# Kernel tuning notes

Measured on AMD Instinct MI355X. Metric: run time of the kernel, lower is better.

Reference implementation:

```python
import jax, jax.numpy as jnp
import numpy as np

N = 64
DX0 = np.pi / N
B = 4096
N_ENV = 8
CODE = 128


def setup_inputs() -> dict:
    key = jax.random.key(0)
    k1, k2, k3 = jax.random.split(key, 3)
    y0 = jax.random.normal(k1, (B, 1, N, N), dtype=jnp.float32)
    env = jax.random.randint(k2, (B,), 0, N_ENV).astype(jnp.int64)
    codes = jax.random.normal(k3, (B, CODE), dtype=jnp.float32)
    t = jnp.zeros((1,), dtype=jnp.float32)
    # learned params: [mu, domain_placeholder] per env (matches nn.Parameter init)
    params = jnp.concatenate([jnp.full((N_ENV, 1), 0.005, jnp.float32),
                              jnp.full((N_ENV, 1), 1.0, jnp.float32)], axis=1)
    # fixed domain buffer for n_env == 8
    domain = jnp.array([0.75, 1.0, 0.75, 1.0, 0.75, 1.0, 0.75, 1.0],
                       dtype=jnp.float32)[:, None]  # [n_env, 1]
    return {"t": t, "y0": y0, "env": env, "codes": codes,
            "params": params, "domain": domain}


def _dx(a):  # roll along last axis (torch dims=2 on [B,H,W])
    return jnp.roll(a, -1, axis=2) - jnp.roll(a, 1, axis=2)


def _dy(a):  # roll along axis 1
    return jnp.roll(a, -1, axis=1) - jnp.roll(a, 1, axis=1)


def _laplacian2d(a, fdx2):
    # torch conv2d (cross-correlation) with kernel [[0,1,0],[1,-4,1],[1,1,0]]
    # and circular padding; note the asymmetric bottom row (faithful to source).
    lap = (jnp.roll(a, 1, axis=1)                    # a[i-1, j]
           + jnp.roll(a, 1, axis=2)                  # a[i, j-1]
           - 4.0 * a
           + jnp.roll(a, -1, axis=2)                 # a[i, j+1]
           + jnp.roll(jnp.roll(a, -1, axis=1), 1, axis=2)  # a[i+1, j-1]
           + jnp.roll(a, -1, axis=1))                # a[i+1, j]
    return lap / fdx2


def _poisson_solve(w, fdx):
    # w: [B,N,N]; fdx: [B,1] grid spacing per sample
    w_pad = jnp.pad(w, ((0, 0), (0, 1), (0, 1)), mode='wrap')  # [B,N+1,N+1]
    wf = jnp.fft.fft2(w_pad / (N ** 2))
    base = jnp.fft.fftfreq(N + 1).astype(w.dtype)       # fftfreq(n, d) = base / d
    k = (2.0 * np.pi) * base[None, :] / fdx             # [B, N+1]
    k2 = k[:, :, None] ** 2 + k[:, None, :] ** 2        # [B, N+1, N+1]
    uf = -wf / (1e-12 + k2)
    uf = uf.at[:, 0, 0].set(0.0)
    return jnp.fft.ifft2((N ** 2) * uf).real[:, :N, :N]


def reference(t, y0, env, codes, params, domain):
    x = y0[:, 0]                              # [B,N,N]
    p = params[env]                           # [B,2]
    mu = p[:, 0:1][..., None]                 # [B,1,1]
    fdx = domain[env] * DX0                   # [B,1]
    psi = _poisson_solve(-x, fdx)             # [B,N,N]
    fdx2 = (fdx[..., None]) ** 2              # [B,1,1]

    rxm = jnp.roll(x, -1, axis=2); rxp = jnp.roll(x, 1, axis=2)
    rym = jnp.roll(x, -1, axis=1); ryp = jnp.roll(x, 1, axis=1)
    pxm = jnp.roll(psi, -1, axis=2); pxp = jnp.roll(psi, 1, axis=2)
    pym = jnp.roll(psi, -1, axis=1); pyp = jnp.roll(psi, 1, axis=1)

    J1 = (_dy(psi) * _dx(x) - _dx(psi) * _dy(x)) / (4.0 * fdx2)
    J2 = (rxm * _dy(pxm) - rxp * _dy(pxp)
          - rym * _dx(pym) + ryp * _dx(pyp)) / (4.0 * fdx2)
    J3 = (jnp.roll(rxm, -1, axis=1) * (pym - pxm)
          - jnp.roll(rxp, 1, axis=1) * (pxp - pyp)
          - jnp.roll(rxp, -1, axis=1) * (pym - pxp)
          + jnp.roll(rxm, 1, axis=1) * (pxm - pyp)) / (4.0 * fdx2)

    dudt = -(J1 + J2 + J3) / 3.0 + mu * _laplacian2d(x, fdx2)
    return dudt[:, None]                      # [B,1,N,N]
```

## Files before the change

### kernel.cpp

```cpp
#include <hip/hip_runtime.h>
#include <math.h>


typedef _Float16 half8 __attribute__((ext_vector_type(8)));
typedef _Float16 half4 __attribute__((ext_vector_type(4)));
typedef float floatx4 __attribute__((ext_vector_type(4)));

#define WPI 0.09666439165562847f

#define H_TB1 0
#define H_TA2 10240
#define H_TG  20480
#define H_TH  26624
#define F_GR32 16384
#define F_GI32 16432
#define F_HC32 16480
#define F_HS32 16528
#define F_SE   16576
#define F_SEG  (F_SE + 264)

__device__ __forceinline__ float trig65(int t, int isSin) {
    return isSin ? __sinf(WPI * (float)t) : __cosf(WPI * (float)t);
}

__global__ void setup_tables(float* __restrict__ ws, const float* __restrict__ domain) {
    int idx = blockIdx.x * 256 + threadIdx.x;
    _Float16* tbH = (_Float16*)ws;
    const float inv = 1.0f / 4225.0f;
    if (idx < 32768) {
        float v = 0.0f;
        int part;
        if (idx < 10240) {
            int chunk = idx >> 9, within = idx & 511;
            part = chunk & 1; int kc = (chunk >> 1) & 1, ni = chunk >> 2;
            int l2 = within >> 3, j = within & 7;
            int row = 16 * ni + (l2 & 15);
            int k = 32 * kc + 8 * (l2 >> 4) + j;
            if (row < 66) {
                int c = (row < 32) ? row : (row < 64 ? row - 32 : 32);
                int isS = (row < 32) ? 0 : (row < 64 ? 1 : row - 64);
                v = trig65((k * c) % 65, isS);
                if (k == 0) v += trig65((64 * c) % 65, isS);
            }
        } else if (idx < 20480) {
            int i2 = idx - 10240;
            int chunk = i2 >> 9, within = i2 & 511;
            part = chunk & 1; int kc = (chunk >> 1) & 1, mi = chunk >> 2;
            int l2 = within >> 3, j = within & 7;
            int row = 16 * mi + (l2 & 15);
            int m = 32 * kc + 8 * (l2 >> 4) + j;
            if (row < 66) {
                int jr = (row < 32) ? row : (row < 64 ? row - 32 : 32);
                int isS = (row < 32) ? 0 : (row < 64 ? 1 : row - 64);
                float s = isS ? 1.0f : -1.0f;
                v = s * trig65((jr * m) % 65, isS);
                if (m == 0) v += s * trig65((jr * 64) % 65, isS);
            }
        } else if (idx < 26624) {
            int i2 = idx - 20480;
            int chunk = i2 >> 9, within = i2 & 511;
            part = chunk & 1; int g = (chunk >> 1) & 1, si = chunk >> 2;
            int l2 = within >> 3, j = within & 7;
            int s = 16 * si + (l2 & 15);
            int jj = 8 * (l2 >> 4) + j;
            if (s <= 32) v = trig65((s * jj) % 65, g);
        } else {
            int i2 = idx - 26624;
            int chunk = i2 >> 9, within = i2 & 511;
            part = chunk & 1; int h = (chunk >> 1) & 1, pi2 = chunk >> 2;
            int l2 = within >> 3, j = within & 7;
            int p = 16 * pi2 + (l2 & 15);
            int c = 8 * (l2 >> 4) + j;
            if (p <= 32) {
                if (c == 0) v = h ? 0.0f : inv;
                else v = 2.0f * inv * trig65((c * p) % 65, h);
            }
        }
        _Float16 hh = (_Float16)v;
        tbH[idx] = part ? (_Float16)(v - (float)hh) : hh;
    } else if (idx < 32960) {
        int i2 = idx - 32768;
        int grp = i2 / 48, s = i2 - grp * 48;
        float v = 0.0f;
        if (s <= 32) {
            int t = (32 * s) % 65;
            float cs = __cosf(WPI * t), sn = __sinf(WPI * t);
            v = (grp == 0) ? cs : (grp == 1) ? sn : (grp == 2) ? 2.0f * inv * cs : 2.0f * inv * sn;
        }
        ws[F_GR32 + i2] = v;
    } else if (idx < 41672) {
        int i2 = idx - 32960;
        const float DX0 = 0.04908738521234052f;
        int e2, a, b2;
        if (i2 < 264) {
            e2 = i2 / 33; a = i2 - e2 * 33; b2 = 32;
        } else {
            int i3 = i2 - 264;
            e2 = i3 / 1056;
            int rem = i3 - e2 * 1056;
            a = rem >> 5; b2 = rem & 31;
        }
        float fdx = domain[e2] * DX0;
        float tt = 6.283185307179586f / (65.0f * fdx);
        float s2v = tt * tt;
        ws[F_SE + i2] = -1.0f / (1e-12f + s2v * (float)(a * a + b2 * b2));
    }
}

#define MFMA16(A, B, C) __builtin_amdgcn_mfma_f32_16x16x32_f16((A), (B), (C), 0, 0, 0)

__global__ __launch_bounds__(512, 8)
void turb_kernel(const float* __restrict__ y0, const int* __restrict__ env,
                 const float* __restrict__ params, const float* __restrict__ domain,
                 const float* __restrict__ ws, float* __restrict__ out) {
    __shared__ __align__(16) char lds_raw[40448];
    _Float16* Yt  = (_Float16*)lds_raw;
    _Float16* Xr  = (_Float16*)lds_raw;
    _Float16* Xi  = (_Float16*)(lds_raw + 9216);
    float*    X32r = (float*)(lds_raw + 18432);
    float*    X32i = (float*)(lds_raw + 18688);
    _Float16* ST  = (_Float16*)(lds_raw + 18944);
    float*    S32 = (float*)(lds_raw + 18944 + 19008);
    float*    psiT = (float*)(lds_raw + 18944);

    const int b = blockIdx.x, tid = threadIdx.x;
    const int wid = __builtin_amdgcn_readfirstlane(tid >> 6);
    const int lane = tid & 63, n16 = lane & 15, q = lane >> 4;
    const int lane8 = lane * 8;
    const int e = __builtin_amdgcn_readfirstlane(env[b]);
    const _Float16* tbH = (const _Float16*)ws;
    const float* tf = ws;
    const float* Se3 = tf + F_SE + e * 33;
    const float* Seg = tf + F_SEG + e * 1056;
    const float* x0 = y0 + (size_t)b * 4096;

    const float DX0 = 0.04908738521234052f;
    const float mu = params[2 * e];
    const float fdx = domain[e] * DX0;
    const float fdx2 = fdx * fdx;
    const float inv12 = 1.0f / (12.0f * fdx2);
    const float invf = mu / fdx2;

    {
        const int mi = wid & 3;
        half8 Ah[2], Al[2];
        const float* xrow = x0 + (16 * mi + n16) * 64 + 8 * q;
        #pragma unroll
        for (int kc = 0; kc < 2; kc++) {
            float4 v0 = *(const float4*)(xrow + 32 * kc);
            float4 v1 = *(const float4*)(xrow + 32 * kc + 4);
            float vv[8] = {v0.x, v0.y, v0.z, v0.w, v1.x, v1.y, v1.z, v1.w};
            #pragma unroll
            for (int u = 0; u < 8; u++) {
                _Float16 h = (_Float16)vv[u];
                Ah[kc][u] = h; Al[kc][u] = (_Float16)(vv[u] - (float)h);
            }
        }
        const int niBeg = (wid & 4) ? 3 : 0;
        const int niEnd = (wid & 4) ? 5 : 3;
        for (int ni = niBeg; ni < niEnd; ni++) {
            const _Float16* tb = tbH + H_TB1 + ni * 2048 + lane8;
            half8 B0h = *(const half8*)(tb);
            half8 B0l = *(const half8*)(tb + 512);
            half8 B1h = *(const half8*)(tb + 1024);
            half8 B1l = *(const half8*)(tb + 1536);
            floatx4 acc = {0.f, 0.f, 0.f, 0.f};
            acc = MFMA16(Ah[0], B0h, acc); acc = MFMA16(Ah[0], B0l, acc); acc = MFMA16(Al[0], B0h, acc);
            acc = MFMA16(Ah[1], B1h, acc); acc = MFMA16(Ah[1], B1l, acc); acc = MFMA16(Al[1], B1h, acc);
            int cp = 16 * ni + n16;
            if (ni < 4 || n16 < 2) {
                half4 hh, ll;
                #pragma unroll
                for (int i = 0; i < 4; i++) {
                    _Float16 h = (_Float16)acc[i];
                    hh[i] = h; ll[i] = (_Float16)(acc[i] - (float)h);
                }
                *(half4*)(Yt + cp * 136 + 16 * mi + 4 * q) = hh;
                *(half4*)(Yt + cp * 136 + 64 + 16 * mi + 4 * q) = ll;
            }
        }
    }
    __syncthreads();

    {
        int pos = wid;
        half8 Ah0, Al0, Ah1, Al1;
        {
            const _Float16* ta = tbH + H_TA2 + (pos / 5) * 2048 + lane8;
            Ah0 = *(const half8*)(ta);
            Al0 = *(const half8*)(ta + 512);
            Ah1 = *(const half8*)(ta + 1024);
            Al1 = *(const half8*)(ta + 1536);
        }
        while (pos < 25) {
            const int mi = pos / 5, ni = pos - 5 * mi;
            const int npos = pos + 8;
            half8 nAh0 = {}, nAl0 = {}, nAh1 = {}, nAl1 = {};
            if (npos < 25) {
                const _Float16* ta = tbH + H_TA2 + (npos / 5) * 2048 + lane8;
                nAh0 = *(const half8*)(ta);
                nAl0 = *(const half8*)(ta + 512);
                nAh1 = *(const half8*)(ta + 1024);
                nAl1 = *(const half8*)(ta + 1536);
            }
            const _Float16* yrow = Yt + (16 * ni + n16) * 136 + 8 * q;
            half8 Bh0 = *(const half8*)(yrow);
            half8 Bl0 = *(const half8*)(yrow + 64);
            half8 Bh1 = *(const half8*)(yrow + 32);
            half8 Bl1 = *(const half8*)(yrow + 96);
            floatx4 acc = {0.f, 0.f, 0.f, 0.f};
            acc = MFMA16(Ah0, Bh0, acc); acc = MFMA16(Ah0, Bl0, acc); acc = MFMA16(Al0, Bh0, acc);
            acc = MFMA16(Ah1, Bh1, acc); acc = MFMA16(Ah1, Bl1, acc); acc = MFMA16(Al1, Bh1, acc);
            if ((ni < 4) || (n16 < 2)) {
                int cp = 16 * ni + n16;
                int cc = (ni == 4) ? 32 : (cp & 31);
                int isS = (ni == 4) ? n16 : (ni >> 1);
                if (mi < 4) {
                    int isQ = mi >> 1;
                    int sid = isQ ? (isS ? 3 : 1) : (isS ? 2 : 0);
                    int jjb = 16 * (mi & 1) + 4 * q;
                    floatx4 Sv = *(const floatx4*)(Seg + cc * 32 + jjb);
                    float ssg = (sid == 2) ? -2.0f : 2.0f;
                    half4 hh, ll;
                    #pragma unroll
                    for (int i = 0; i < 4; i++) {
                        float v = ssg * Sv[i] * acc[i];
                        _Float16 h = (_Float16)v;
                        hh[i] = h; ll[i] = (_Float16)(v - (float)h);
                    }
                    _Float16* sb = ST + sid * 2376 + cc * 72 + jjb;
                    *(half4*)sb = hh;
                    *(half4*)(sb + 32) = ll;
                } else if (q == 0) {
                    float S = Se3[cc];
                    #pragma unroll
                    for (int i = 0; i < 2; i++) {
                        int sid = i ? (isS ? 3 : 1) : (isS ? 2 : 0);
                        float v = 2.0f * S * acc[i];
                        if (sid == 2) v = -v;
                        S32[sid * 36 + cc] = v;
                    }
                }
            }
            Ah0 = nAh0; Al0 = nAl0; Ah1 = nAh1; Al1 = nAl1;
            pos = npos;
        }
    }
    __syncthreads();

    if (tid < 33) {
        int c = tid;
        float v0[4];
        #pragma unroll
        for (int sid = 0; sid < 4; sid++)
            v0[sid] = (float)ST[sid * 2376 + c * 72] + (float)ST[sid * 2376 + c * 72 + 32];
        float pr = 0.5f * (v0[0] + v0[3]), pi = 0.5f * (v0[1] + v0[2]);
        if (c == 0) { pr = 0.f; pi = 0.f; }
        float outs[4] = {pr, pi, pi, pr};
        #pragma unroll
        for (int sid = 0; sid < 4; sid++) {
            _Float16 h = (_Float16)outs[sid];
            ST[sid * 2376 + c * 72] = h;
            ST[sid * 2376 + c * 72 + 32] = (_Float16)(outs[sid] - (float)h);
        }
    }
    __syncthreads();

    for (int pos = wid; pos < 18; pos += 8) {
        const int ci = pos / 6, rem = pos - 6 * ci;
        const int si = rem >> 1, g = rem & 1;
        const _Float16* st0 = ST + (2 * g) * 2376 + (16 * ci + n16) * 72 + 8 * q;
        half8 A0h = *(const half8*)(st0),        A0l = *(const half8*)(st0 + 32);
        half8 A1h = *(const half8*)(st0 + 2376), A1l = *(const half8*)(st0 + 2376 + 32);
        const _Float16* tg = tbH + H_TG + si * 2048 + lane8;
        half8 Grh = *(const half8*)(tg);
        half8 Grl = *(const half8*)(tg + 512);
        half8 Gih = *(const half8*)(tg + 1024);
        half8 Gil = *(const half8*)(tg + 1536);
        floatx4 aA = {0.f,0.f,0.f,0.f}, aB = aA;
        aA = MFMA16(A0h, Grh, aA); aA = MFMA16(A0h, Grl, aA); aA = MFMA16(A0l, Grh, aA);
        aB = MFMA16(A1h, Gih, aB); aB = MFMA16(A1h, Gil, aB); aB = MFMA16(A1l, Gih, aB);
        int s = 16 * si + n16;
        float ga = tf[F_GR32 + s], gi2 = tf[F_GI32 + s];
        bool sval = (si < 2) || (n16 == 0);
        _Float16* Xo = g ? Xi : Xr;
        float* X32o = g ? X32i : X32r;
        const float sgn = g ? 1.0f : -1.0f;
        if (ci < 2) {
            const int cb = 16 * ci + 4 * q;
            floatx4 U0 = *(const floatx4*)(S32 + (2 * g) * 36 + cb);
            floatx4 U1 = *(const floatx4*)(S32 + (2 * g + 1) * 36 + cb);
            half4 hP, lP, hM, lM;
            #pragma unroll
            for (int i = 0; i < 4; i++) {
                float av = aA[i] + ga * U0[i], bv = aB[i] + gi2 * U1[i];
                float xP = av + sgn * bv;
                float xM = av - sgn * bv;
                _Float16 h;
                h = (_Float16)xP; hP[i] = h; lP[i] = (_Float16)(xP - (float)h);
                h = (_Float16)xM; hM[i] = h; lM[i] = (_Float16)(xM - (float)h);
            }
            if (sval) {
                *(half4*)(Xo + s * 72 + cb) = hP;  *(half4*)(Xo + s * 72 + 32 + cb) = lP;
                if (s >= 2) {
                    int sm = 65 - s;
                    *(half4*)(Xo + sm * 72 + cb) = hM;  *(half4*)(Xo + sm * 72 + 32 + cb) = lM;
                }
            }
        } else if (q == 0 && sval) {
            float u0 = S32[(2 * g) * 36 + 32], u1 = S32[(2 * g + 1) * 36 + 32];
            float av = aA[0] + ga * u0, bv = aB[0] + gi2 * u1;
            X32o[s] = av + sgn * bv;
            if (s >= 2) X32o[65 - s] = av - sgn * bv;
        }
    }
    __syncthreads();

    for (int pos = wid; pos < 12; pos += 8) {
        const int ri = pos / 3, pti = pos - 3 * ri;
        const int brow = (16 * ri + n16) * 72 + 8 * q;
        half8 Brh = *(const half8*)(Xr + brow), Brl = *(const half8*)(Xr + brow + 32);
        half8 Bih = *(const half8*)(Xi + brow), Bil = *(const half8*)(Xi + brow + 32);
        const _Float16* th = tbH + H_TH + pti * 2048 + lane8;
        half8 Hch = *(const half8*)(th);
        half8 Hcl = *(const half8*)(th + 512);
        half8 Hsh = *(const half8*)(th + 1024);
        half8 Hsl = *(const half8*)(th + 1536);
        floatx4 aE = {0.f,0.f,0.f,0.f}, aF = aE;
        aE = MFMA16(Hch, Brh, aE); aE = MFMA16(Hch, Brl, aE); aE = MFMA16(Hcl, Brh, aE);
        aF = MFMA16(Hsh, Bih, aF); aF = MFMA16(Hsh, Bil, aF); aF = MFMA16(Hsl, Bih, aF);
        int r = 16 * ri + n16;
        float xr32 = X32r[r], xi32 = X32i[r];
        if (pti < 2) {
            const int pb = 16 * pti + 4 * q;
            floatx4 Hc4 = *(const floatx4*)(tf + F_HC32 + pb);
            floatx4 Hs4 = *(const floatx4*)(tf + F_HS32 + pb);
            float* pp = psiT + pb * 65 + r;
            float* pm = psiT + (65 - pb) * 65 + r;
            #pragma unroll
            for (int i = 0; i < 4; i++) {
                float E = aE[i] + xr32 * Hc4[i];
                float F = aF[i] + xi32 * Hs4[i];
                pp[i * 65] = E - F;
                if (pb + i >= 2) pm[-i * 65] = E + F;
            }
        } else if (q == 0) {
            float E = aE[0] + xr32 * tf[F_HC32 + 32];
            float F = aF[0] + xi32 * tf[F_HS32 + 32];
            psiT[32 * 65 + r] = E - F;
            psiT[33 * 65 + r] = E + F;
        }
    }
    __syncthreads();

    {
        const int c = lane;
        const int cm1 = (c + 63) & 63, cp1 = (c + 1) & 63;
        const int r0 = wid * 8;
        const float* xL = x0 + r0 * 64 + cm1;
        const float* xC = x0 + r0 * 64 + c;
        const float* xR = x0 + r0 * 64 + cp1;
        const float* pL = psiT + cm1 * 65 + r0;
        const float* pC = psiT + c * 65 + r0;
        const float* pR = psiT + cp1 * 65 + r0;
        float* ob = out + (size_t)b * 4096 + r0 * 64 + c;
        const int mo = (wid == 0) ? 63 : -1;
        float xLm = xL[mo * 64], xCm = xC[mo * 64], xRm = xR[mo * 64];
        float pLm = pL[mo], pCm = pC[mo], pRm = pR[mo];
        float xLc = xL[0], xCc = xC[0], xRc = xR[0];
        float pLc = pL[0], pCc = pC[0], pRc = pR[0];
        #pragma unroll
        for (int it = 0; it < 8; it++) {
            int ro = it + 1;
            if (it == 7 && wid == 7) ro = -56;
            float xLp = xL[ro * 64], xCp = xC[ro * 64], xRp = xR[ro * 64];
            float pLp = pL[ro], pCp = pC[ro], pRp = pR[ro];
            float J1 = (pCp - pCm) * (xRc - xLc) - (pRc - pLc) * (xCp - xCm);
            float J2 = xRc * (pRp - pRm) - xLc * (pLp - pLm) - xCp * (pRp - pLp) + xCm * (pRm - pLm);
            float J3 = xRp * (pCp - pRc) - xLm * (pLc - pCm) - xLp * (pCp - pLc) + xRm * (pRc - pCm);
            float lap = xCm + xLc - 4.f * xCc + xRc + xLp + xCp;
            ob[it * 64] = -(J1 + J2 + J3) * inv12 + lap * invf;
            xLm = xLc; xCm = xCc; xRm = xRc; pLm = pLc; pCm = pCc; pRm = pRc;
            xLc = xLp; xCc = xCp; xRc = xRp; pLc = pLp; pCc = pCp; pRc = pRp;
        }
    }
}

extern "C" void kernel_launch(void* const* d_in, const int* in_sizes, int n_in,
                              void* d_out, int out_size, void* d_ws, size_t ws_size,
                              hipStream_t stream) {
    const float* y0     = (const float*)d_in[1];
    const int*   env    = (const int*)d_in[2];
    const float* params = (const float*)d_in[4];
    const float* domain = (const float*)d_in[5];
    float* out = (float*)d_out;
    float* ws  = (float*)d_ws;

    setup_tables<<<dim3(163), dim3(256), 0, stream>>>(ws, domain);
    turb_kernel<<<dim3(4096), dim3(512), 0, stream>>>(y0, env, params, domain, ws, out);
}
```

Measured before the change: 185.3 us.

## Process two samples per block, sharing twiddle table fragments across both

Each block now handles two batch samples, each with its own LDS arena, and the grid is halved. Table operands (DFT matrices) loaded from global memory are reused for both samples' MFMA chains, and the 4-stage pipeline gets more MFMA work per barrier. This doubles LDS use per block to about 80KB and lowers launch bounds to 4 blocks per CU, so occupancy drops. Register pressure also rises because A fragments for two samples are held at once.

Result: faster. 179.9 us (-2.9%).

```diff
diff --git a/kernel.cpp b/kernel.cpp
--- a/kernel.cpp
+++ b/kernel.cpp
@@ -18,6 +18,16 @@
 #define F_HS32 16528
 #define F_SE   16576
 #define F_SEG  (F_SE + 264)
+
+#define ARENA 40448
+#define OFF_YT   0
+#define OFF_XR   0
+#define OFF_XI   9216
+#define OFF_X32R 18432
+#define OFF_X32I 18688
+#define OFF_ST   18944
+#define OFF_S32  37952
+#define OFF_PSIT 18944
 
 __device__ __forceinline__ float trig65(int t, int isSin) {
     return isSin ? __sinf(WPI * (float)t) : __cosf(WPI * (float)t);
@@ -92,9 +102,8 @@
         int i2 = idx - 32960;
         const float DX0 = 0.04908738521234052f;
         int e2, a, b2;
-        if (i2 < 264) {
-            e2 = i2 / 33; a = i2 - e2 * 33; b2 = 32;
-        } else {
+        if (i2 < 264) { e2 = i2 / 33; a = i2 - e2 * 33; b2 = 32; }
+        else {
             int i3 = i2 - 264;
             e2 = i3 / 1056;
             int rem = i3 - e2 * 1056;
@@ -109,51 +118,51 @@
 
 #define MFMA16(A, B, C) __builtin_amdgcn_mfma_f32_16x16x32_f16((A), (B), (C), 0, 0, 0)
 
-__global__ __launch_bounds__(512, 8)
+__global__ __launch_bounds__(512, 4)
 void turb_kernel(const float* __restrict__ y0, const int* __restrict__ env,
                  const float* __restrict__ params, const float* __restrict__ domain,
                  const float* __restrict__ ws, float* __restrict__ out) {
-    __shared__ __align__(16) char lds_raw[40448];
-    _Float16* Yt  = (_Float16*)lds_raw;
-    _Float16* Xr  = (_Float16*)lds_raw;
-    _Float16* Xi  = (_Float16*)(lds_raw + 9216);
-    float*    X32r = (float*)(lds_raw + 18432);
-    float*    X32i = (float*)(lds_raw + 18688);
-    _Float16* ST  = (_Float16*)(lds_raw + 18944);
-    float*    S32 = (float*)(lds_raw + 18944 + 19008);
-    float*    psiT = (float*)(lds_raw + 18944);
-
-    const int b = blockIdx.x, tid = threadIdx.x;
+    __shared__ __align__(16) char lds_raw[2 * ARENA];
+
+    const int b0 = blockIdx.x * 2, tid = threadIdx.x;
     const int wid = __builtin_amdgcn_readfirstlane(tid >> 6);
     const int lane = tid & 63, n16 = lane & 15, q = lane >> 4;
     const int lane8 = lane * 8;
-    const int e = __builtin_amdgcn_readfirstlane(env[b]);
     const _Float16* tbH = (const _Float16*)ws;
     const float* tf = ws;
-    const float* Se3 = tf + F_SE + e * 33;
-    const float* Seg = tf + F_SEG + e * 1056;
-    const float* x0 = y0 + (size_t)b * 4096;
-
+
+    const int eA0 = __builtin_amdgcn_readfirstlane(env[b0]);
+    const int eA1 = __builtin_amdgcn_readfirstlane(env[b0 + 1]);
+    const float* SegA[2] = {tf + F_SEG + eA0 * 1056, tf + F_SEG + eA1 * 1056};
+    const float* Se3A[2] = {tf + F_SE + eA0 * 33,   tf + F_SE + eA1 * 33};
+    const float* xA[2]   = {y0 + (size_t)b0 * 4096,  y0 + (size_t)(b0 + 1) * 4096};
+    float* outA[2]       = {out + (size_t)b0 * 4096, out + (size_t)(b0 + 1) * 4096};
     const float DX0 = 0.04908738521234052f;
-    const float mu = params[2 * e];
-    const float fdx = domain[e] * DX0;
-    const float fdx2 = fdx * fdx;
-    const float inv12 = 1.0f / (12.0f * fdx2);
-    const float invf = mu / fdx2;
+    float invfA[2], inv12A[2];
+    {
+        float mu0 = params[2 * eA0], mu1 = params[2 * eA1];
+        float f0 = domain[eA0] * DX0, f1 = domain[eA1] * DX0;
+        float f02 = f0 * f0, f12 = f1 * f1;
+        inv12A[0] = 1.0f / (12.0f * f02); invfA[0] = mu0 / f02;
+        inv12A[1] = 1.0f / (12.0f * f12); invfA[1] = mu1 / f12;
+    }
 
     {
         const int mi = wid & 3;
-        half8 Ah[2], Al[2];
-        const float* xrow = x0 + (16 * mi + n16) * 64 + 8 * q;
-        #pragma unroll
-        for (int kc = 0; kc < 2; kc++) {
-            float4 v0 = *(const float4*)(xrow + 32 * kc);
-            float4 v1 = *(const float4*)(xrow + 32 * kc + 4);
-            float vv[8] = {v0.x, v0.y, v0.z, v0.w, v1.x, v1.y, v1.z, v1.w};
+        half8 Ah[2][2], Al[2][2];
+        #pragma unroll
+        for (int t = 0; t < 2; t++) {
+            const float* xrow = xA[t] + (16 * mi + n16) * 64 + 8 * q;
             #pragma unroll
-            for (int u = 0; u < 8; u++) {
-                _Float16 h = (_Float16)vv[u];
-                Ah[kc][u] = h; Al[kc][u] = (_Float16)(vv[u] - (float)h);
+            for (int kc = 0; kc < 2; kc++) {
+                float4 v0 = *(const float4*)(xrow + 32 * kc);
+                float4 v1 = *(const float4*)(xrow + 32 * kc + 4);
+                float vv[8] = {v0.x, v0.y, v0.z, v0.w, v1.x, v1.y, v1.z, v1.w};
+                #pragma unroll
+                for (int u = 0; u < 8; u++) {
+                    _Float16 h = (_Float16)vv[u];
+                    Ah[t][kc][u] = h; Al[t][kc][u] = (_Float16)(vv[u] - (float)h);
+                }
             }
         }
         const int niBeg = (wid & 4) ? 3 : 0;
@@ -164,46 +173,45 @@
             half8 B0l = *(const half8*)(tb + 512);
             half8 B1h = *(const half8*)(tb + 1024);
             half8 B1l = *(const half8*)(tb + 1536);
-            floatx4 acc = {0.f, 0.f, 0.f, 0.f};
-            acc = MFMA16(Ah[0], B0h, acc); acc = MFMA16(Ah[0], B0l, acc); acc = MFMA16(Al[0], B0h, acc);
-            acc = MFMA16(Ah[1], B1h, acc); acc = MFMA16(Ah[1], B1l, acc); acc = MFMA16(Al[1], B1h, acc);
-            int cp = 16 * ni + n16;
-            if (ni < 4 || n16 < 2) {
-                half4 hh, ll;
-                #pragma unroll
-                for (int i = 0; i < 4; i++) {
-                    _Float16 h = (_Float16)acc[i];
-                    hh[i] = h; ll[i] = (_Float16)(acc[i] - (float)h);
+            const int cp = 16 * ni + n16;
+            const bool st = (ni < 4 || n16 < 2);
+            #pragma unroll
+            for (int t = 0; t < 2; t++) {
+                floatx4 acc = {0.f, 0.f, 0.f, 0.f};
+                acc = MFMA16(Ah[t][0], B0h, acc); acc = MFMA16(Ah[t][0], B0l, acc); acc = MFMA16(Al[t][0], B0h, acc);
+                acc = MFMA16(Ah[t][1], B1h, acc); acc = MFMA16(Ah[t][1], B1l, acc); acc = MFMA16(Al[t][1], B1h, acc);
+                if (st) {
+                    half4 hh, ll;
+                    #pragma unroll
+                    for (int i = 0; i < 4; i++) {
+                        _Float16 h = (_Float16)acc[i];
+                        hh[i] = h; ll[i] = (_Float16)(acc[i] - (float)h);
+                    }
+                    _Float16* Yt = (_Float16*)(lds_raw + t * ARENA + OFF_YT);
+                    *(half4*)(Yt + cp * 136 + 16 * mi + 4 * q) = hh;
+                    *(half4*)(Yt + cp * 136 + 64 + 16 * mi + 4 * q) = ll;
                 }
-                *(half4*)(Yt + cp * 136 + 16 * mi + 4 * q) = hh;
-                *(half4*)(Yt + cp * 136 + 64 + 16 * mi + 4 * q) = ll;
             }
         }
     }
     __syncthreads();
 
-    {
-        int pos = wid;
-        half8 Ah0, Al0, Ah1, Al1;
-        {
-            const _Float16* ta = tbH + H_TA2 + (pos / 5) * 2048 + lane8;
-            Ah0 = *(const half8*)(ta);
-            Al0 = *(const half8*)(ta + 512);
-            Ah1 = *(const half8*)(ta + 1024);
-            Al1 = *(const half8*)(ta + 1536);
-        }
-        while (pos < 25) {
-            const int mi = pos / 5, ni = pos - 5 * mi;
-            const int npos = pos + 8;
-            half8 nAh0 = {}, nAl0 = {}, nAh1 = {}, nAl1 = {};
-            if (npos < 25) {
-                const _Float16* ta = tbH + H_TA2 + (npos / 5) * 2048 + lane8;
-                nAh0 = *(const half8*)(ta);
-                nAl0 = *(const half8*)(ta + 512);
-                nAh1 = *(const half8*)(ta + 1024);
-                nAl1 = *(const half8*)(ta + 1536);
-            }
-            const _Float16* yrow = Yt + (16 * ni + n16) * 136 + 8 * q;
+    for (int pos = wid; pos < 25; pos += 8) {
+        const int mi = pos / 5, ni = pos - 5 * mi;
+        const _Float16* ta = tbH + H_TA2 + mi * 2048 + lane8;
+        half8 Ah0 = *(const half8*)(ta);
+        half8 Al0 = *(const half8*)(ta + 512);
+        half8 Ah1 = *(const half8*)(ta + 1024);
+        half8 Al1 = *(const half8*)(ta + 1536);
+        const int yoff = (16 * ni + n16) * 136 + 8 * q;
+        const int cp = 16 * ni + n16;
+        const int cc = (ni == 4) ? 32 : (cp & 31);
+        const int isS = (ni == 4) ? n16 : (ni >> 1);
+        const bool valid = (ni < 4) || (n16 < 2);
+        #pragma unroll
+        for (int t = 0; t < 2; t++) {
+            const _Float16* Yt = (const _Float16*)(lds_raw + t * ARENA + OFF_YT);
+            const _Float16* yrow = Yt + yoff;
             half8 Bh0 = *(const half8*)(yrow);
             half8 Bl0 = *(const half8*)(yrow + 64);
             half8 Bh1 = *(const half8*)(yrow + 32);
@@ -211,15 +219,14 @@
             floatx4 acc = {0.f, 0.f, 0.f, 0.f};
             acc = MFMA16(Ah0, Bh0, acc); acc = MFMA16(Ah0, Bl0, acc); acc = MFMA16(Al0, Bh0, acc);
             acc = MFMA16(Ah1, Bh1, acc); acc = MFMA16(Ah1, Bl1, acc); acc = MFMA16(Al1, Bh1, acc);
-            if ((ni < 4) || (n16 < 2)) {
-                int cp = 16 * ni + n16;
-                int cc = (ni == 4) ? 32 : (cp & 31);
-                int isS = (ni == 4) ? n16 : (ni >> 1);
+            if (valid) {
+                _Float16* ST = (_Float16*)(lds_raw + t * ARENA + OFF_ST);
+                float* S32 = (float*)(lds_raw + t * ARENA + OFF_S32);
                 if (mi < 4) {
-                    int isQ = mi >> 1;
-                    int sid = isQ ? (isS ? 3 : 1) : (isS ? 2 : 0);
-                    int jjb = 16 * (mi & 1) + 4 * q;
-                    floatx4 Sv = *(const floatx4*)(Seg + cc * 32 + jjb);
+                    const int isQ = mi >> 1;
+                    const int sid = isQ ? (isS ? 3 : 1) : (isS ? 2 : 0);
+                    const int jjb = 16 * (mi & 1) + 4 * q;
+                    floatx4 Sv = *(const floatx4*)(SegA[t] + cc * 32 + jjb);
                     float ssg = (sid == 2) ? -2.0f : 2.0f;
                     half4 hh, ll;
                     #pragma unroll
@@ -232,7 +239,7 @@
                     *(half4*)sb = hh;
                     *(half4*)(sb + 32) = ll;
                 } else if (q == 0) {
-                    float S = Se3[cc];
+                    float S = Se3A[t][cc];
                     #pragma unroll
                     for (int i = 0; i < 2; i++) {
                         int sid = i ? (isS ? 3 : 1) : (isS ? 2 : 0);
@@ -242,14 +249,13 @@
                     }
                 }
             }
-            Ah0 = nAh0; Al0 = nAl0; Ah1 = nAh1; Al1 = nAl1;
-            pos = npos;
         }
     }
     __syncthreads();
 
-    if (tid < 33) {
-        int c = tid;
+    if (wid < 2 && lane < 33) {
+        _Float16* ST = (_Float16*)(lds_raw + wid * ARENA + OFF_ST);
+        const int c = lane;
         float v0[4];
         #pragma unroll
         for (int sid = 0; sid < 4; sid++)
@@ -269,55 +275,69 @@
     for (int pos = wid; pos < 18; pos += 8) {
         const int ci = pos / 6, rem = pos - 6 * ci;
         const int si = rem >> 1, g = rem & 1;
-        const _Float16* st0 = ST + (2 * g) * 2376 + (16 * ci + n16) * 72 + 8 * q;
-        half8 A0h = *(const half8*)(st0),        A0l = *(const half8*)(st0 + 32);
-        half8 A1h = *(const half8*)(st0 + 2376), A1l = *(const half8*)(st0 + 2376 + 32);
         const _Float16* tg = tbH + H_TG + si * 2048 + lane8;
         half8 Grh = *(const half8*)(tg);
         half8 Grl = *(const half8*)(tg + 512);
         half8 Gih = *(const half8*)(tg + 1024);
         half8 Gil = *(const half8*)(tg + 1536);
-        floatx4 aA = {0.f,0.f,0.f,0.f}, aB = aA;
-        aA = MFMA16(A0h, Grh, aA); aA = MFMA16(A0h, Grl, aA); aA = MFMA16(A0l, Grh, aA);
-        aB = MFMA16(A1h, Gih, aB); aB = MFMA16(A1h, Gil, aB); aB = MFMA16(A1l, Gih, aB);
-        int s = 16 * si + n16;
-        float ga = tf[F_GR32 + s], gi2 = tf[F_GI32 + s];
-        bool sval = (si < 2) || (n16 == 0);
-        _Float16* Xo = g ? Xi : Xr;
-        float* X32o = g ? X32i : X32r;
+        const int s = 16 * si + n16;
+        const float ga = tf[F_GR32 + s], gi2 = tf[F_GI32 + s];
+        const bool sval = (si < 2) || (n16 == 0);
         const float sgn = g ? 1.0f : -1.0f;
-        if (ci < 2) {
-            const int cb = 16 * ci + 4 * q;
-            floatx4 U0 = *(const floatx4*)(S32 + (2 * g) * 36 + cb);
-            floatx4 U1 = *(const floatx4*)(S32 + (2 * g + 1) * 36 + cb);
-            half4 hP, lP, hM, lM;
-            #pragma unroll
-            for (int i = 0; i < 4; i++) {
-                float av = aA[i] + ga * U0[i], bv = aB[i] + gi2 * U1[i];
-                float xP = av + sgn * bv;
-                float xM = av - sgn * bv;
-                _Float16 h;
-                h = (_Float16)xP; hP[i] = h; lP[i] = (_Float16)(xP - (float)h);
-                h = (_Float16)xM; hM[i] = h; lM[i] = (_Float16)(xM - (float)h);
-            }
-            if (sval) {
-                *(half4*)(Xo + s * 72 + cb) = hP;  *(half4*)(Xo + s * 72 + 32 + cb) = lP;
-                if (s >= 2) {
-                    int sm = 65 - s;
-                    *(half4*)(Xo + sm * 72 + cb) = hM;  *(half4*)(Xo + sm * 72 + 32 + cb) = lM;
+        const int cb = 16 * ci + 4 * q;
+        const int aoff = (2 * g) * 2376 + (16 * ci + n16) * 72 + 8 * q;
+        #pragma unroll
+        for (int t = 0; t < 2; t++) {
+            const _Float16* ST = (const _Float16*)(lds_raw + t * ARENA + OFF_ST);
+            const float* S32 = (const float*)(lds_raw + t * ARENA + OFF_S32);
+            const _Float16* st0 = ST + aoff;
+            half8 A0h = *(const half8*)(st0),        A0l = *(const half8*)(st0 + 32);
+            half8 A1h = *(const half8*)(st0 + 2376), A1l = *(const half8*)(st0 + 2376 + 32);
+            floatx4 aA = {0.f,0.f,0.f,0.f}, aB = aA;
+            aA = MFMA16(A0h, Grh, aA); aA = MFMA16(A0h, Grl, aA); aA = MFMA16(A0l, Grh, aA);
+            aB = MFMA16(A1h, Gih, aB); aB = MFMA16(A1h, Gil, aB); aB = MFMA16(A1l, Gih, aB);
+            _Float16* Xo = (_Float16*)(lds_raw + t * ARENA + (g ? OFF_XI : OFF_XR));
+            float* X32o = (float*)(lds_raw + t * ARENA + (g ? OFF_X32I : OFF_X32R));
+            if (ci < 2) {
+                floatx4 U0 = *(const floatx4*)(S32 + (2 * g) * 36 + cb);
+                floatx4 U1 = *(const floatx4*)(S32 + (2 * g + 1) * 36 + cb);
+                half4 hP, lP, hM, lM;
+                #pragma unroll
+                for (int i = 0; i < 4; i++) {
+                    float av = aA[i] + ga * U0[i], bv = aB[i] + gi2 * U1[i];
+                    float xP = av + sgn * bv;
+                    float xM = av - sgn * bv;
+                    _Float16 h;
+                    h = (_Float16)xP; hP[i] = h; lP[i] = (_Float16)(xP - (float)h);
+                    h = (_Float16)xM; hM[i] = h; lM[i] = (_Float16)(xM - (float)h);
                 }
-            }
-        } else if (q == 0 && sval) {
-            float u0 = S32[(2 * g) * 36 + 32], u1 = S32[(2 * g + 1) * 36 + 32];
-            float av = aA[0] + ga * u0, bv = aB[0] + gi2 * u1;
-            X32o[s] = av + sgn * bv;
-            if (s >= 2) X32o[65 - s] = av - sgn * bv;
+                if (sval) {
+                    *(half4*)(Xo + s * 72 + cb) = hP;  *(half4*)(Xo + s * 72 + 32 + cb) = lP;
+                    if (s >= 2) {
+                        int sm = 65 - s;
+                        *(half4*)(Xo + sm * 72 + cb) = hM;  *(half4*)(Xo + sm * 72 + 32 + cb) = lM;
+                    }
+                }
+            } else if (q == 0 && sval) {
+                float u0 = S32[(2 * g) * 36 + 32], u1 = S32[(2 * g + 1) * 36 + 32];
+                float av = aA[0] + ga * u0, bv = aB[0] + gi2 * u1;
+                X32o[s] = av + sgn * bv;
+                if (s >= 2) X32o[65 - s] = av - sgn * bv;
+            }
         }
     }
     __syncthreads();
 
-    for (int pos = wid; pos < 12; pos += 8) {
+    for (int p24 = wid; p24 < 24; p24 += 8) {
+        const int t = p24 / 12;
+        const int pos = p24 - 12 * t;
         const int ri = pos / 3, pti = pos - 3 * ri;
+        const char* base = lds_raw + t * ARENA;
+        const _Float16* Xr = (const _Float16*)(base + OFF_XR);
+        const _Float16* Xi = (const _Float16*)(base + OFF_XI);
+        const float* X32r = (const float*)(base + OFF_X32R);
+        const float* X32i = (const float*)(base + OFF_X32I);
+        float* psiT = (float*)(base + OFF_PSIT);
         const int brow = (16 * ri + n16) * 72 + 8 * q;
         half8 Brh = *(const half8*)(Xr + brow), Brl = *(const half8*)(Xr + brow + 32);
         half8 Bih = *(const half8*)(Xi + brow), Bil = *(const half8*)(Xi + brow + 32);
@@ -329,7 +349,7 @@
         floatx4 aE = {0.f,0.f,0.f,0.f}, aF = aE;
         aE = MFMA16(Hch, Brh, aE); aE = MFMA16(Hch, Brl, aE); aE = MFMA16(Hcl, Brh, aE);
         aF = MFMA16(Hsh, Bih, aF); aF = MFMA16(Hsh, Bil, aF); aF = MFMA16(Hsl, Bih, aF);
-        int r = 16 * ri + n16;
+        const int r = 16 * ri + n16;
         float xr32 = X32r[r], xi32 = X32i[r];
         if (pti < 2) {
             const int pb = 16 * pti + 4 * q;
@@ -353,7 +373,11 @@
     }
     __syncthreads();
 
-    {
+    #pragma unroll
+    for (int t = 0; t < 2; t++) {
+        const float* psiT = (const float*)(lds_raw + t * ARENA + OFF_PSIT);
+        const float* x0 = xA[t];
+        const float inv12 = inv12A[t], invf = invfA[t];
         const int c = lane;
         const int cm1 = (c + 63) & 63, cp1 = (c + 1) & 63;
         const int r0 = wid * 8;
@@ -363,7 +387,7 @@
         const float* pL = psiT + cm1 * 65 + r0;
         const float* pC = psiT + c * 65 + r0;
         const float* pR = psiT + cp1 * 65 + r0;
-        float* ob = out + (size_t)b * 4096 + r0 * 64 + c;
+        float* ob = outA[t] + r0 * 64 + c;
         const int mo = (wid == 0) ? 63 : -1;
         float xLm = xL[mo * 64], xCm = xC[mo * 64], xRm = xR[mo * 64];
         float pLm = pL[mo], pCm = pC[mo], pRm = pR[mo];
@@ -397,5 +421,5 @@
     float* ws  = (float*)d_ws;
 
     setup_tables<<<dim3(163), dim3(256), 0, stream>>>(ws, domain);
-    turb_kernel<<<dim3(4096), dim3(512), 0, stream>>>(y0, env, params, domain, ws, out);
+    turb_kernel<<<dim3(2048), dim3(512), 0, stream>>>(y0, env, params, domain, ws, out);
 }
```
